# Kernel tuning notes

Measured on AMD Instinct MI355X. Metric: run time of the kernel, lower is better.

The kernel has to match this reference:

```python
import jax, jax.numpy as jnp
import numpy as np
from jax import lax

TAU = 2.0      # LIF decay constant (source: tau = 2.0)
V_TH = 1.0     # spikingjelly LIFNode default threshold
ALPHA = 2.0    # ATan surrogate default alpha
BN_EPS = 1e-5


@jax.custom_vjp
def spike(v):
    # Heaviside with ATan surrogate gradient (spikingjelly surrogate.ATan)
    return (v >= V_TH).astype(v.dtype)

def _spike_fwd(v):
    return spike(v), v

def _spike_bwd(v, g):
    x = (jnp.pi / 2.0) * ALPHA * (v - V_TH)
    return (g * (ALPHA / 2.0) / (1.0 + x * x),)

spike.defvjp(_spike_fwd, _spike_bwd)


def lif_step(v, x):
    # leaky integrate: v += (x - (v - v_reset)) / tau, v_reset = 0
    v = v + (x - v) / TAU
    s = spike(v)
    # hard reset to 0; detach_reset=True -> stop_gradient on s in the reset path
    v = v * (1.0 - lax.stop_gradient(s))
    return v, s


def multistep_lif(x_seq):
    # x_seq: (T, ...) ; membrane state carried across T, initial v = 0
    v0 = jnp.zeros_like(x_seq[0])
    _, s_seq = lax.scan(lif_step, v0, x_seq)
    return s_seq


def setup_inputs() -> dict:
    key = jax.random.key(0)
    ks = jax.random.split(key, 3)
    bs, length, c_num, hidden = 64, 128, 32, 256
    x = jax.random.normal(ks[0], (bs, length, c_num), dtype=jnp.float32)
    conv_w = jax.random.normal(ks[1], (hidden, 1, 1, 3), dtype=jnp.float32) * 0.3
    conv_b = jnp.zeros((hidden,), jnp.float32)
    bn_gamma = jnp.ones((hidden,), jnp.float32)
    bn_beta = jnp.zeros((hidden,), jnp.float32)
    bn_mean = jnp.zeros((hidden,), jnp.float32)
    bn_var = jnp.ones((hidden,), jnp.float32)
    lin_w = jax.random.normal(ks[2], (hidden, hidden), dtype=jnp.float32) * (1.0 / np.sqrt(hidden))
    lin_b = jnp.zeros((hidden,), jnp.float32)
    return {"x": x, "conv_w": conv_w, "conv_b": conv_b, "bn_gamma": bn_gamma,
            "bn_beta": bn_beta, "bn_mean": bn_mean, "bn_var": bn_var,
            "lin_w": lin_w, "lin_b": lin_b}


def reference(x, conv_w, conv_b, bn_gamma, bn_beta, bn_mean, bn_var, lin_w, lin_b):
    bs, length, c_num = x.shape
    hidden = conv_w.shape[0]

    # ---- ConvEncoder ----
    xi = jnp.transpose(x, (0, 2, 1))[:, None]  # (bs, 1, c_num, length)
    enc = lax.conv_general_dilated(
        xi, conv_w, window_strides=(1, 1), padding=((0, 0), (1, 1)),
        dimension_numbers=("NCHW", "OIHW", "NCHW"))
    enc = enc + conv_b[None, :, None, None]
    # BatchNorm2d (eval mode, running stats)
    inv = bn_gamma * lax.rsqrt(bn_var + BN_EPS)
    enc = (enc - bn_mean[None, :, None, None]) * inv[None, :, None, None] + bn_beta[None, :, None, None]
    # multi-step LIF over channel dim T = hidden (as in source permute(1,0,2,3))
    enc = jnp.transpose(enc, (1, 0, 2, 3))          # (hidden, bs, c_num, length)
    spks_enc = multistep_lif(enc)                   # (hidden, bs, c_num, length)

    # ---- reshape to per-(bs*c_num) sequences of length `length` with feature hidden ----
    h = jnp.transpose(spks_enc, (1, 2, 3, 0)).reshape(bs * c_num, length, hidden)

    # ---- SpikeRNNCell recurrence over time (Linear + stateful LIF) ----
    def rnn_step(v, x_t):                           # x_t: (N, hidden)
        z = x_t @ lin_w.T + lin_b
        v = v + (z - v) / TAU
        s = spike(v)
        v = v * (1.0 - lax.stop_gradient(s))
        return v, s

    v0 = jnp.zeros((bs * c_num, hidden), x.dtype)
    _, s_seq = lax.scan(rnn_step, v0, jnp.transpose(h, (1, 0, 2)))  # (length, N, hidden)
    spks = s_seq[-1]                                # final-step spikes (N, hidden)

    spks = spks.reshape(bs, c_num * hidden, -1)     # (bs, c_num*hidden, 1)
    return jnp.transpose(spks, (0, 2, 1)), spks[:, :, -1]
```

## Files before the change

kernel.cpp:

```cpp
#include <hip/hip_runtime.h>
#include <stdint.h>

typedef unsigned short u16;
typedef unsigned int u32;
typedef unsigned long long u64;
typedef unsigned char u8;

typedef __attribute__((ext_vector_type(4))) int   i32x4;
typedef __attribute__((ext_vector_type(8))) int   i32x8;
typedef __attribute__((ext_vector_type(4))) float f32x4;
typedef __attribute__((ext_vector_type(2))) float f32x2;

#define OFF_SBITS 0u
#define SBITS_BYTES (2048u * 128u * 32u)
#define OFF_WQ4  (SBITS_BYTES)
#define WQ4_BYTES (2u * 32768u)
#define OFF_SCL  (OFF_WQ4 + WQ4_BYTES)

__device__ __forceinline__ f32x2 pk_fma(f32x2 a, f32x2 b, f32x2 c) {
    f32x2 d;
    asm("v_pk_fma_f32 %0, %1, %2, %3"
        : "=v"(d) : "v"(a), "v"(b), "v"(c));
    return d;
}
__device__ __forceinline__ f32x2 pk_fma_lw(f32x2 a, f32x2 b) {
    f32x2 d;
    asm("v_pk_fma_f32 %0, %1, %2, %1 op_sel:[0,0,1] op_sel_hi:[0,1,1]"
        : "=v"(d) : "v"(a), "v"(b));
    return d;
}
__device__ __forceinline__ f32x2 pk_fma_b11(f32x2 a, f32x2 b, f32x2 c) {
    f32x2 d;
    asm("v_pk_fma_f32 %0, %1, %2, %3 op_sel:[1,0,0] op_sel_hi:[1,1,1]"
        : "=v"(d) : "v"(a), "v"(b), "v"(c));
    return d;
}
__device__ __forceinline__ f32x2 pk_fma_b00(f32x2 a, f32x2 b, f32x2 c) {
    f32x2 d;
    asm("v_pk_fma_f32 %0, %1, %2, %3 op_sel:[0,0,0] op_sel_hi:[0,1,1]"
        : "=v"(d) : "v"(a), "v"(b), "v"(c));
    return d;
}

__global__ __launch_bounds__(256) void prep_enc_kernel(
    const float* __restrict__ x,
    const float* __restrict__ conv_w, const float* __restrict__ conv_b,
    const float* __restrict__ gamma,  const float* __restrict__ beta,
    const float* __restrict__ mean,   const float* __restrict__ var,
    const float* __restrict__ lin_w,  uint8_t* __restrict__ ws,
    u32* __restrict__ sbits) {
    int tid = threadIdx.x;
    int blk = blockIdx.x;
    if (blk < 256) {
        __shared__ float red[256];
        __shared__ u8 nib[256];
        int j = blk, k = tid;
        float wv = lin_w[j * 256 + k];
        red[k] = fabsf(wv);
        __syncthreads();
        #pragma unroll
        for (int s = 128; s > 0; s >>= 1) {
            if (k < s) red[k] = fmaxf(red[k], red[k + s]);
            __syncthreads();
        }
        float m = red[0];
        float S = (m > 0.f) ? 6.0f / m : 0.f;
        float v6 = wv * S;
        float av = fabsf(v6);
        int code;
        if      (av < 0.25f) code = 0;
        else if (av < 0.75f) code = 1;
        else if (av < 1.25f) code = 2;
        else if (av < 1.75f) code = 3;
        else if (av < 2.5f)  code = 4;
        else if (av < 3.5f)  code = 5;
        else if (av < 5.0f)  code = 6;
        else                 code = 7;
        nib[k] = (u8)(((v6 < 0.f && code) ? 8 : 0) | code);
        __syncthreads();
        if (k < 128) {
            u8 byte = (u8)(nib[2 * k] | (nib[2 * k + 1] << 4));
            int ks = k >> 6, kb = (k >> 4) & 3, bi = k & 15;
            (ws + OFF_WQ4)[ks * 32768 + (j * 4 + kb) * 16 + bi] = byte;
        }
        if (k == 0) ((float*)(ws + OFF_SCL))[j] = m * (1.0f / 12.0f);
    } else {
        __shared__ f32x4 cfl[256];
        {
            int h = tid;
            float inv = gamma[h] / sqrtf(var[h] + 1e-5f);
            float K = (conv_b[h] - mean[h]) * inv + beta[h];
            f32x4 cc = {conv_w[h * 3 + 0] * inv * 0.5f,
                        conv_w[h * 3 + 1] * inv * 0.5f,
                        conv_w[h * 3 + 2] * inv * 0.5f, K * 0.5f};
            cfl[h] = cc;
        }
        int p = (blk - 256) * 256 + tid;
        int l = p & 127;
        int c = (p >> 7) & 31;
        int b0 = p >> 12;
        int xb = b0 * 4096 + l * 32 + c;
        float xb0 = x[xb],            xb1 = x[xb + 131072];
        float xa0 = (l > 0)   ? x[xb - 32]          : 0.f;
        float xa1 = (l > 0)   ? x[xb + 131072 - 32] : 0.f;
        float xc0 = (l < 127) ? x[xb + 32]          : 0.f;
        float xc1 = (l < 127) ? x[xb + 131072 + 32] : 0.f;
        u32* d0 = sbits + (size_t)(b0 * 32 + c) * 1024 + l;
        u32* d1 = d0 + (size_t)1024 * 1024;

        f32x2 XA = {xa0, xa1};
        f32x2 XB = {xb0, xb1};
        f32x2 XC = {xc0, xc1};
        const f32x2 hf2 = {0.5f, 0.5f};

        __syncthreads();
        f32x2 v2 = {0.f, 0.f};
        #pragma unroll 1
        for (int hc = 0; hc < 8; ++hc) {
            u32 c0 = 0, c1 = 0;
            #pragma unroll
            for (int k = 0; k < 32; ++k) {
                f32x4 a4 = cfl[hc * 32 + k];
                f32x2 p0 = __builtin_shufflevector(a4, a4, 0, 1);
                f32x2 p1 = __builtin_shufflevector(a4, a4, 2, 3);
                f32x2 e = pk_fma_lw(p1, XC);
                e = pk_fma_b11(p0, XB, e);
                e = pk_fma_b00(p0, XA, e);
                v2 = pk_fma(hf2, v2, e);
                bool s0 = (v2.x >= 1.0f);
                bool s1 = (v2.y >= 1.0f);
                c0 = (c0 << 1) | (u32)s0;
                c1 = (c1 << 1) | (u32)s1;
                v2.x = s0 ? 0.f : v2.x;
                v2.y = s1 ? 0.f : v2.y;
            }
            d0[hc * 128] = __builtin_bitreverse32(c0);
            d1[hc * 128] = __builtin_bitreverse32(c1);
        }
    }
}

__device__ __forceinline__ u32 nib_perm(u32 byte) {
    u32 t1 = byte | (byte << 6);
    u32 t2 = t1 | (t1 << 12);
    u32 sel = t2 & 0x03030303u;
    return __builtin_amdgcn_perm(0x22200200u, 0x22200200u, sel);
}

__global__ __launch_bounds__(256, 2) void gemm_scan_kernel(
    const u32* __restrict__ sbits,
    const uint4* __restrict__ wq4,
    const float* __restrict__ lin_b,
    const float* __restrict__ sclp,
    float* __restrict__ out) {
    __shared__ __align__(16) uint8_t smem[36864];
    u32* Awords = (u32*)smem;

    int tid  = threadIdx.x;
    int n    = blockIdx.x;
    int lane = tid & 63;
    int w    = tid >> 6;
    int l15  = lane & 15;
    int quad = lane >> 4;
    int lb   = w * 256 + l15 * 4 + quad;

    float bias = lin_b[tid];
    float sc   = sclp[tid];

    i32x4 bb[2][4];
    #pragma unroll
    for (int ks = 0; ks < 2; ++ks)
        #pragma unroll
        for (int nf = 0; nf < 4; ++nf)
            bb[ks][nf] = ((const i32x4*)wq4)[(size_t)(ks * 2048 + nf * 64 + lb)];

    __builtin_amdgcn_global_load_lds(
        (const __attribute__((address_space(1))) u32*)
            (sbits + (size_t)n * 1024 + tid * 4),
        (__attribute__((address_space(3))) u32*)(smem + w * 1024), 16, 0, 0);

    f32x4 acc[8][4];
    #pragma unroll
    for (int mf = 0; mf < 8; ++mf)
        #pragma unroll
        for (int nf = 0; nf < 4; ++nf) {
            f32x4 z = {0.f, 0.f, 0.f, 0.f};
            acc[mf][nf] = z;
        }

    __syncthreads();

    u32 aw[8][2];
    #pragma unroll
    for (int mf = 0; mf < 8; ++mf)
        #pragma unroll
        for (int ks = 0; ks < 2; ++ks)
            aw[mf][ks] = Awords[(ks * 4 + quad) * 128 + mf * 16 + l15];

    __syncthreads();

    i32x8 afr;
    afr[4] = 0; afr[5] = 0; afr[6] = 0; afr[7] = 0;

    #pragma unroll
    for (int ks = 0; ks < 2; ++ks) {
        i32x8 bfr[4];
        #pragma unroll
        for (int nf = 0; nf < 4; ++nf) {
            bfr[nf][0] = bb[ks][nf][0]; bfr[nf][1] = bb[ks][nf][1];
            bfr[nf][2] = bb[ks][nf][2]; bfr[nf][3] = bb[ks][nf][3];
            bfr[nf][4] = 0; bfr[nf][5] = 0; bfr[nf][6] = 0; bfr[nf][7] = 0;
        }
        #pragma unroll
        for (int mf = 0; mf < 8; ++mf) {
            u32 wbits = aw[mf][ks];
            afr[0] = (int)nib_perm(wbits & 0xFFu);
            afr[1] = (int)nib_perm((wbits >> 8) & 0xFFu);
            afr[2] = (int)nib_perm((wbits >> 16) & 0xFFu);
            afr[3] = (int)nib_perm(wbits >> 24);
            #pragma unroll
            for (int nf = 0; nf < 4; ++nf) {
                acc[mf][nf] = __builtin_amdgcn_mfma_scale_f32_16x16x128_f8f6f4(
                    afr, bfr[nf], acc[mf][nf], 4, 4,
                    0, 0x7F7F7F7F, 0, 0x7F7F7F7F);
            }
        }
    }

    float* ZW = (float*)(smem + (size_t)w * 9216);
    float zsc = sc;
    float zbi = 0.5f * bias;
    float v = 0.f, sOut = 0.f;
    #pragma unroll
    for (int ph = 0; ph < 4; ++ph) {
        #pragma unroll
        for (int mm = 0; mm < 2; ++mm) {
            int mf = ph * 2 + mm;
            #pragma unroll
            for (int nf = 0; nf < 4; ++nf)
                *(f32x4*)(ZW + (nf * 16 + l15) * 36 + mm * 16 + quad * 4) =
                    acc[mf][nf];
        }
        float zh[32];
        #pragma unroll
        for (int g = 0; g < 8; ++g) {
            f32x4 z4 = *(const f32x4*)(ZW + lane * 36 + g * 4);
            #pragma unroll
            for (int r = 0; r < 4; ++r)
                zh[g * 4 + r] = fmaf(z4[r], zsc, zbi);
        }
        #pragma unroll
        for (int tl = 0; tl < 32; ++tl) {
            v = fmaf(0.5f, v, zh[tl]);
            bool s = (v >= 1.0f);
            if (ph == 3 && tl == 31) sOut = s ? 1.f : 0.f;
            v = s ? 0.f : v;
        }
    }
    out[(size_t)n * 256 + tid]           = sOut;
    out[524288u + (size_t)n * 256 + tid] = sOut;
}

extern "C" void kernel_launch(void* const* d_in, const int* in_sizes, int n_in,
                              void* d_out, int out_size, void* d_ws, size_t ws_size,
                              hipStream_t stream) {
    const float* x      = (const float*)d_in[0];
    const float* conv_w = (const float*)d_in[1];
    const float* conv_b = (const float*)d_in[2];
    const float* gamma  = (const float*)d_in[3];
    const float* beta   = (const float*)d_in[4];
    const float* mean   = (const float*)d_in[5];
    const float* var    = (const float*)d_in[6];
    const float* lin_w  = (const float*)d_in[7];
    const float* lin_b  = (const float*)d_in[8];
    uint8_t* ws = (uint8_t*)d_ws;
    float* out = (float*)d_out;

    hipLaunchKernelGGL(prep_enc_kernel, dim3(768), dim3(256), 0, stream,
                       x, conv_w, conv_b, gamma, beta, mean, var, lin_w,
                       ws, (u32*)(ws + OFF_SBITS));
    hipLaunchKernelGGL(gemm_scan_kernel, dim3(2048), dim3(256), 0, stream,
                       (const u32*)(ws + OFF_SBITS),
                       (const uint4*)(ws + OFF_WQ4), lin_b,
                       (const float*)(ws + OFF_SCL), out);
}
```

Before: 109.5 us.

## Pre-expand spike nibbles into LDS once and rescale LIF recurrence domain

The A-operand bit-to-FP4 expansion, previously recomputed per lane for every m-fragment, is now done once cooperatively into a padded LDS region and read back as 16-byte vectors before the MFMAs. The LIF scan also moves into the raw accumulator domain, folding scale and bias into a per-channel threshold and reset value, which removes one FMA per timestep and the staging zh array. This trades ALU work for LDS capacity (shared memory rises to about 53KB, which may cut occupancy below two blocks per CU) and adds extra LDS traffic. The rescaled threshold comparison can round differently from the original formulation.

```diff
diff --git a/kernel.cpp b/kernel.cpp
--- a/kernel.cpp
+++ b/kernel.cpp
@@ -147,13 +147,15 @@
     return __builtin_amdgcn_perm(0x22200200u, 0x22200200u, sel);
 }
 
+#define EXP_OFF 36864
+
 __global__ __launch_bounds__(256, 2) void gemm_scan_kernel(
     const u32* __restrict__ sbits,
     const uint4* __restrict__ wq4,
     const float* __restrict__ lin_b,
     const float* __restrict__ sclp,
     float* __restrict__ out) {
-    __shared__ __align__(16) uint8_t smem[36864];
+    __shared__ __align__(16) uint8_t smem[53760];
     u32* Awords = (u32*)smem;
 
     int tid  = threadIdx.x;
@@ -165,7 +167,9 @@
     int lb   = w * 256 + l15 * 4 + quad;
 
     float bias = lin_b[tid];
-    float sc   = sclp[tid];
+    float zscg = fmaxf(sclp[tid], 1e-37f);
+    float uth  = (1.0f - bias) / zscg;
+    float urst = (0.0f - bias) / zscg;
 
     i32x4 bb[2][4];
     #pragma unroll
@@ -190,17 +194,23 @@
 
     __syncthreads();
 
-    u32 aw[8][2];
-    #pragma unroll
-    for (int mf = 0; mf < 8; ++mf)
-        #pragma unroll
-        for (int ks = 0; ks < 2; ++ks)
-            aw[mf][ks] = Awords[(ks * 4 + quad) * 128 + mf * 16 + l15];
+    #pragma unroll
+    for (int j = 0; j < 4; ++j) {
+        int wi = tid + 256 * j;
+        u32 wv = Awords[wi];
+        int hc = wi >> 7, l = wi & 127;
+        int ks = hc >> 2, q = hc & 3;
+        i32x4 ex;
+        ex[0] = (int)nib_perm(wv & 0xFFu);
+        ex[1] = (int)nib_perm((wv >> 8) & 0xFFu);
+        ex[2] = (int)nib_perm((wv >> 16) & 0xFFu);
+        ex[3] = (int)nib_perm(wv >> 24);
+        *(i32x4*)(smem + EXP_OFF + ((l * 33 + ks * 16 + q * 4) << 2)) = ex;
+    }
 
     __syncthreads();
 
-    i32x8 afr;
-    afr[4] = 0; afr[5] = 0; afr[6] = 0; afr[7] = 0;
+    const uint8_t* expB = smem + EXP_OFF + ((l15 * 33 + quad * 4) << 2);
 
     #pragma unroll
     for (int ks = 0; ks < 2; ++ks) {
@@ -213,11 +223,10 @@
         }
         #pragma unroll
         for (int mf = 0; mf < 8; ++mf) {
-            u32 wbits = aw[mf][ks];
-            afr[0] = (int)nib_perm(wbits & 0xFFu);
-            afr[1] = (int)nib_perm((wbits >> 8) & 0xFFu);
-            afr[2] = (int)nib_perm((wbits >> 16) & 0xFFu);
-            afr[3] = (int)nib_perm(wbits >> 24);
+            i32x4 a4 = *(const i32x4*)(expB + ks * 64 + mf * 2112);
+            i32x8 afr;
+            afr[0] = a4[0]; afr[1] = a4[1]; afr[2] = a4[2]; afr[3] = a4[3];
+            afr[4] = 0; afr[5] = 0; afr[6] = 0; afr[7] = 0;
             #pragma unroll
             for (int nf = 0; nf < 4; ++nf) {
                 acc[mf][nf] = __builtin_amdgcn_mfma_scale_f32_16x16x128_f8f6f4(
@@ -228,9 +237,7 @@
     }
 
     float* ZW = (float*)(smem + (size_t)w * 9216);
-    float zsc = sc;
-    float zbi = 0.5f * bias;
-    float v = 0.f, sOut = 0.f;
+    float u = urst, sOut = 0.f;
     #pragma unroll
     for (int ph = 0; ph < 4; ++ph) {
         #pragma unroll
@@ -241,20 +248,16 @@
                 *(f32x4*)(ZW + (nf * 16 + l15) * 36 + mm * 16 + quad * 4) =
                     acc[mf][nf];
         }
-        float zh[32];
         #pragma unroll
         for (int g = 0; g < 8; ++g) {
             f32x4 z4 = *(const f32x4*)(ZW + lane * 36 + g * 4);
             #pragma unroll
-            for (int r = 0; r < 4; ++r)
-                zh[g * 4 + r] = fmaf(z4[r], zsc, zbi);
-        }
-        #pragma unroll
-        for (int tl = 0; tl < 32; ++tl) {
-            v = fmaf(0.5f, v, zh[tl]);
-            bool s = (v >= 1.0f);
-            if (ph == 3 && tl == 31) sOut = s ? 1.f : 0.f;
-            v = s ? 0.f : v;
+            for (int r = 0; r < 4; ++r) {
+                u = fmaf(0.5f, u, z4[r]);
+                bool s = (u >= uth);
+                if (ph == 3 && g == 7 && r == 3) sOut = s ? 1.f : 0.f;
+                u = s ? urst : u;
+            }
         }
     }
     out[(size_t)n * 256 + tid]           = sOut;
```

Measured after the change: 119.3 us. 1.09x slower.
